# Kernel optimization log

Measured on AMD Instinct MI355X. Metric: run time of the kernel, lower is better.

## Reference

```python
import jax, jax.numpy as jnp
import numpy as np

B, N = 16, 512          # graphs, nodes per graph (equal-size dynamic batch)
IN, HID, OUT, K = 256, 128, 256, 16  # hidden = in_dim // red_factor
EPS = 1e-5


def setup_inputs() -> dict:
    key = jax.random.key(0)
    ks = jax.random.split(key, 12)
    def lin(k, fi, fo):
        return jax.random.normal(k, (fi, fo), jnp.float32) / np.sqrt(fi).astype(np.float32)
    return {
        "obj_encs": jax.random.normal(ks[0], (B * N, IN), jnp.float32),
        "n_nodes": jnp.full((B,), N, dtype=jnp.int32),
        # self-graph-attention params (in -> hidden), with residual projection
        "Wq": lin(ks[1], IN, HID), "bq": jnp.zeros((HID,), jnp.float32),
        "Wk": lin(ks[2], IN, HID), "bk": jnp.zeros((HID,), jnp.float32),
        "Wv": lin(ks[3], IN, HID), "bv": jnp.zeros((HID,), jnp.float32),
        "Wr": lin(ks[4], IN, HID), "br": jnp.zeros((HID,), jnp.float32),
        # EdgeConv (local+global => 2*HID input features)
        "Wc": lin(ks[5], 2 * HID, OUT), "bc": jnp.zeros((OUT,), jnp.float32),
        # LayerNorm affine
        "ln_scale": jnp.ones((OUT,), jnp.float32),
        "ln_bias": jnp.zeros((OUT,), jnp.float32),
    }


def _forward(obj_encs, n_nodes, Wq, bq, Wk, bk, Wv, bv, Wr, br, Wc, bc, ln_scale, ln_bias):
    # dynamic batching: equal-size graphs per n_nodes -> reshape [B, N, IN]
    x = obj_encs.reshape(B, N, IN)

    # --- SelfGraphAttentionLinear (per-graph dot-product attention, residual) ---
    q = x @ Wq + bq                      # [B, N, HID]
    kk = x @ Wk + bk
    v = x @ Wv + bv
    attn = jax.nn.softmax(jnp.einsum('bnd,bmd->bnm', q, kk) / np.sqrt(HID).astype(np.float32), axis=-1)
    h = jnp.einsum('bnm,bmd->bnd', attn, v) + (x @ Wr + br)  # residual projection

    # --- GraphConv: kNN (euclidean) within each graph ---
    sq = jnp.sum(h * h, axis=-1)                             # [B, N]
    dist = sq[:, :, None] + sq[:, None, :] - 2.0 * jnp.einsum('bnd,bmd->bnm', h, h)
    _, idx = jax.lax.top_k(-dist, K)                         # [B, N, K] (self included)

    nb = jax.vmap(lambda hb, ib: hb[ib])(h, idx)             # [B, N, K, HID]
    hc = h[:, :, None, :]                                    # [B, N, 1, HID]
    # features='local+global': [x_i, x_j - x_i]
    e = jnp.concatenate([jnp.broadcast_to(hc, nb.shape), nb - hc], axis=-1)  # [B,N,K,2H]

    y = jnp.einsum('bnkf,fo->bnko', e, Wc) + bc              # [B, N, K, OUT]
    y = jnp.max(y, axis=2)                                   # reduction='max' over k

    mu = jnp.mean(y, axis=-1, keepdims=True)
    var = jnp.mean((y - mu) ** 2, axis=-1, keepdims=True)
    y = (y - mu) / jnp.sqrt(var + EPS) * ln_scale + ln_bias  # LayerNorm
    return jax.nn.selu(y).reshape(B * N, OUT)


def reference(obj_encs, n_nodes, Wq, bq, Wk, bk, Wv, bv, Wr, br, Wc, bc, ln_scale, ln_bias):
    return _forward(obj_encs, n_nodes, Wq, bq, Wk, bk, Wv, bv, Wr, br, Wc, bc, ln_scale, ln_bias)
```

## Files before the change

### kernel.cpp

```cpp
#include <hip/hip_runtime.h>
#include <math.h>

#define NB   16
#define NN   512
#define FIN  256
#define HID  128
#define FOUT 256
#define TOPK 16
#define ROWS (NB*NN)
#define LN_EPS 1e-5f

#define BK  32
#define LDK 40

typedef __attribute__((ext_vector_type(8))) short  bf16x8;
typedef __attribute__((ext_vector_type(4))) float  f32x4;

__device__ __forceinline__ ushort f2bf_rn(float x) {
    uint u = __float_as_uint(x);
    u += 0x7fff + ((u >> 16) & 1);
    return (ushort)(u >> 16);
}
__device__ __forceinline__ float bf2f(ushort h) {
    return __uint_as_float(((uint)h) << 16);
}
__device__ __forceinline__ void split2(float x, ushort& hi, ushort& lo) {
    hi = f2bf_rn(x);
    lo = f2bf_rn(x - bf2f(hi));
}

__device__ __forceinline__ void stage_rows64(ushort (*Dh)[LDK], ushort (*Dl)[LDK],
                                             const float* __restrict__ src,
                                             int rstride, int tid)
{
    const int r = tid >> 2, seg = (tid & 3) * 8;
    const float* p = src + (size_t)r * rstride + seg;
    #pragma unroll
    for (int i = 0; i < 2; i++) {
        const float4 q = *(const float4*)(p + 4*i);
        ushort h0,l0,h1,l1,h2,l2,h3,l3;
        split2(q.x,h0,l0); split2(q.y,h1,l1);
        split2(q.z,h2,l2); split2(q.w,h3,l3);
        *(ushort4*)&Dh[r][seg + 4*i] = make_ushort4(h0,h1,h2,h3);
        *(ushort4*)&Dl[r][seg + 4*i] = make_ushort4(l0,l1,l2,l3);
    }
}

__device__ __forceinline__ void stage_cols64(ushort (*Dh)[LDK], ushort (*Dl)[LDK],
                                             const float* __restrict__ src,
                                             int ldn, int tid)
{
    const int n = tid & 63, kh = (tid >> 6) * 8;
    const float* p = src + (size_t)kh * ldn + n;
    ushort hh[8], ll[8];
    #pragma unroll
    for (int i = 0; i < 8; i++) split2(p[(size_t)i * ldn], hh[i], ll[i]);
    *(ushort4*)&Dh[n][kh]     = make_ushort4(hh[0],hh[1],hh[2],hh[3]);
    *(ushort4*)&Dh[n][kh + 4] = make_ushort4(hh[4],hh[5],hh[6],hh[7]);
    *(ushort4*)&Dl[n][kh]     = make_ushort4(ll[0],ll[1],ll[2],ll[3]);
    *(ushort4*)&Dl[n][kh + 4] = make_ushort4(ll[4],ll[5],ll[6],ll[7]);
}

__device__ __forceinline__ void mma_step64(const ushort (*Ah)[LDK], const ushort (*Al)[LDK],
                                           const ushort (*Bh)[LDK], const ushort (*Bl)[LDK],
                                           f32x4 acc[2][2], int wr, int wc, int lane)
{
    const int q8 = (lane >> 4) * 8, m = lane & 15;
    bf16x8 ah[2], al[2], bh[2], bl[2];
    #pragma unroll
    for (int i = 0; i < 2; i++) {
        ah[i] = *(const bf16x8*)&Ah[wr + 16*i + m][q8];
        al[i] = *(const bf16x8*)&Al[wr + 16*i + m][q8];
        bh[i] = *(const bf16x8*)&Bh[wc + 16*i + m][q8];
        bl[i] = *(const bf16x8*)&Bl[wc + 16*i + m][q8];
    }
    #pragma unroll
    for (int i = 0; i < 2; i++)
        #pragma unroll
        for (int j = 0; j < 2; j++) {
            acc[i][j] = __builtin_amdgcn_mfma_f32_16x16x32_bf16(ah[i], bh[j], acc[i][j], 0, 0, 0);
            acc[i][j] = __builtin_amdgcn_mfma_f32_16x16x32_bf16(ah[i], bl[j], acc[i][j], 0, 0, 0);
            acc[i][j] = __builtin_amdgcn_mfma_f32_16x16x32_bf16(al[i], bh[j], acc[i][j], 0, 0, 0);
        }
}

#define MM64_PROLOGUE()                                                     \
    __shared__ ushort Ah[64][LDK], Al[64][LDK], Bh[64][LDK], Bl[64][LDK];   \
    const int tid = threadIdx.x, lane = tid & 63, wv = tid >> 6;            \
    const int wr = (wv >> 1) * 32, wc = (wv & 1) * 32;                      \
    f32x4 acc[2][2];                                                        \
    _Pragma("unroll")                                                       \
    for (int i = 0; i < 2; i++)                                             \
        _Pragma("unroll")                                                   \
        for (int j = 0; j < 2; j++)                                         \
            acc[i][j] = (f32x4){0.f, 0.f, 0.f, 0.f};

__global__ __launch_bounds__(256) void k_proj_m(
    const float* __restrict__ X,
    const float* __restrict__ Wq, const float* __restrict__ bq,
    const float* __restrict__ Wk, const float* __restrict__ bk,
    const float* __restrict__ Wv, const float* __restrict__ bv,
    const float* __restrict__ Wr, const float* __restrict__ br,
    float* __restrict__ Y)
{
    const int widx = blockIdx.x >> 1;
    const int ch   = (blockIdx.x & 1) * 64;
    const int br0  = blockIdx.y * 64;
    const float* W; const float* bias;
    if      (widx == 0) { W = Wq; bias = bq; }
    else if (widx == 1) { W = Wk; bias = bk; }
    else if (widx == 2) { W = Wv; bias = bv; }
    else                { W = Wr; bias = br; }

    MM64_PROLOGUE();

    for (int k0 = 0; k0 < FIN; k0 += BK) {
        stage_rows64(Ah, Al, X + (size_t)br0 * FIN + k0, FIN, tid);
        stage_cols64(Bh, Bl, W + (size_t)k0 * HID + ch, HID, tid);
        __syncthreads();
        mma_step64(Ah, Al, Bh, Bl, acc, wr, wc, lane);
        __syncthreads();
    }

    const int m = lane & 15, q4 = (lane >> 4) * 4;
    #pragma unroll
    for (int i = 0; i < 2; i++)
        #pragma unroll
        for (int reg = 0; reg < 4; reg++) {
            const int grow = br0 + wr + 16*i + q4 + reg;
            #pragma unroll
            for (int j = 0; j < 2; j++) {
                const int c = ch + wc + 16*j + m;
                Y[(size_t)grow * 512 + widx * 128 + c] = acc[i][j][reg] + bias[c];
            }
        }
}

__global__ __launch_bounds__(256) void k_scores_m(
    const float* __restrict__ Y, float* __restrict__ S)
{
    const int b = blockIdx.z;
    const int m0 = blockIdx.x * 64, n0 = blockIdx.y * 64;
    const float scale = 0.08838834764831845f;
    const float* Yb = Y + (size_t)b * NN * 512;

    MM64_PROLOGUE();

    for (int k0 = 0; k0 < HID; k0 += BK) {
        stage_rows64(Ah, Al, Yb + (size_t)n0 * 512 + k0,       512, tid);
        stage_rows64(Bh, Bl, Yb + (size_t)m0 * 512 + 128 + k0, 512, tid);
        __syncthreads();
        mma_step64(Ah, Al, Bh, Bl, acc, wr, wc, lane);
        __syncthreads();
    }

    float* Sb = S + (size_t)b * NN * NN;
    const int m = lane & 15, q4 = (lane >> 4) * 4;
    #pragma unroll
    for (int i = 0; i < 2; i++)
        #pragma unroll
        for (int reg = 0; reg < 4; reg++) {
            const int n = n0 + wr + 16*i + q4 + reg;
            #pragma unroll
            for (int j = 0; j < 2; j++)
                Sb[(size_t)n * NN + m0 + wc + 16*j + m] = acc[i][j][reg] * scale;
        }
}

__global__ __launch_bounds__(256) void k_softmax(float* __restrict__ S)
{
    float* p = S + (size_t)blockIdx.x * NN;
    const int tid = threadIdx.x;
    const int lane = tid & 63, wave = tid >> 6;
    __shared__ float red[4];

    float v0 = p[tid], v1 = p[tid + 256];
    float mx = fmaxf(v0, v1);
    #pragma unroll
    for (int off = 32; off > 0; off >>= 1) mx = fmaxf(mx, __shfl_down(mx, off));
    if (lane == 0) red[wave] = mx;
    __syncthreads();
    mx = fmaxf(fmaxf(red[0], red[1]), fmaxf(red[2], red[3]));
    __syncthreads();

    float e0 = __expf(v0 - mx), e1 = __expf(v1 - mx);
    float s = e0 + e1;
    #pragma unroll
    for (int off = 32; off > 0; off >>= 1) s += __shfl_down(s, off);
    if (lane == 0) red[wave] = s;
    __syncthreads();
    s = red[0] + red[1] + red[2] + red[3];
    const float inv = 1.0f / s;
    p[tid] = e0 * inv;
    p[tid + 256] = e1 * inv;
}

__global__ __launch_bounds__(256) void k_hgemm_m(
    const float* __restrict__ S, const float* __restrict__ Y,
    float* __restrict__ H)
{
    const int c0 = blockIdx.x * 64;
    const int n0 = blockIdx.y * 64;
    const int b  = blockIdx.z;
    const float* P = S + (size_t)b * NN * NN;

    MM64_PROLOGUE();

    for (int k0 = 0; k0 < NN; k0 += BK) {
        stage_rows64(Ah, Al, P + (size_t)n0 * NN + k0, NN, tid);
        stage_cols64(Bh, Bl, Y + ((size_t)(b * NN + k0)) * 512 + 256 + c0, 512, tid);
        __syncthreads();
        mma_step64(Ah, Al, Bh, Bl, acc, wr, wc, lane);
        __syncthreads();
    }

    const int m = lane & 15, q4 = (lane >> 4) * 4;
    #pragma unroll
    for (int i = 0; i < 2; i++)
        #pragma unroll
        for (int reg = 0; reg < 4; reg++) {
            const int gr = b * NN + n0 + wr + 16*i + q4 + reg;
            #pragma unroll
            for (int j = 0; j < 2; j++) {
                const int c = c0 + wc + 16*j + m;
                H[(size_t)gr * HID + c] = acc[i][j][reg] + Y[(size_t)gr * 512 + 384 + c];
            }
        }
}

__global__ __launch_bounds__(256) void k_sq(
    const float* __restrict__ H, float* __restrict__ SQ)
{
    const int row = blockIdx.x * 4 + (threadIdx.x >> 6);
    const int lane = threadIdx.x & 63;
    float a = H[(size_t)row*HID + lane];
    float c = H[(size_t)row*HID + 64 + lane];
    float s = a*a + c*c;
    #pragma unroll
    for (int off = 32; off > 0; off >>= 1) s += __shfl_down(s, off);
    if (lane == 0) SQ[row] = s;
}

__global__ __launch_bounds__(256) void k_ab_m(
    const float* __restrict__ H, const float* __restrict__ Wc,
    const float* __restrict__ bc, float* __restrict__ AB)
{
    const int ct  = blockIdx.x;
    const int br0 = blockIdx.y * 64;
    const bool bhalf = ct >= 4;
    const int c0 = (ct & 3) * 64;

    MM64_PROLOGUE();

    for (int k0 = 0; k0 < HID; k0 += BK) {
        stage_rows64(Ah, Al, H + (size_t)br0 * HID + k0, HID, tid);
        {
            const int n = tid & 63, kh = (tid >> 6) * 8;
            ushort hh[8], ll[8];
            #pragma unroll
            for (int i = 0; i < 8; i++) {
                const int k = k0 + kh + i;
                const float wbot = Wc[(size_t)(HID + k) * FOUT + c0 + n];
                const float val = bhalf ? wbot
                                        : (Wc[(size_t)k * FOUT + c0 + n] - wbot);
                split2(val, hh[i], ll[i]);
            }
            *(ushort4*)&Bh[n][kh]     = make_ushort4(hh[0],hh[1],hh[2],hh[3]);
            *(ushort4*)&Bh[n][kh + 4] = make_ushort4(hh[4],hh[5],hh[6],hh[7]);
            *(ushort4*)&Bl[n][kh]     = make_ushort4(ll[0],ll[1],ll[2],ll[3]);
            *(ushort4*)&Bl[n][kh + 4] = make_ushort4(ll[4],ll[5],ll[6],ll[7]);
        }
        __syncthreads();
        mma_step64(Ah, Al, Bh, Bl, acc, wr, wc, lane);
        __syncthreads();
    }

    const int m = lane & 15, q4 = (lane >> 4) * 4;
    #pragma unroll
    for (int i = 0; i < 2; i++)
        #pragma unroll
        for (int reg = 0; reg < 4; reg++) {
            const int grow = br0 + wr + 16*i + q4 + reg;
            #pragma unroll
            for (int j = 0; j < 2; j++) {
                const int c = wc + 16*j + m;
                const float add = bhalf ? 0.0f : bc[c0 + c];
                AB[(size_t)grow * 512 + ct * 64 + c] = acc[i][j][reg] + add;
            }
        }
}

__global__ __launch_bounds__(256) void k_dist_m(
    const float* __restrict__ H, const float* __restrict__ SQ,
    float* __restrict__ D)
{
    const int b = blockIdx.z;
    const int m0 = blockIdx.x * 64, n0 = blockIdx.y * 64;
    const float* Hb = H + (size_t)b * NN * HID;

    MM64_PROLOGUE();

    for (int k0 = 0; k0 < HID; k0 += BK) {
        stage_rows64(Ah, Al, Hb + (size_t)n0 * HID + k0, HID, tid);
        stage_rows64(Bh, Bl, Hb + (size_t)m0 * HID + k0, HID, tid);
        __syncthreads();
        mma_step64(Ah, Al, Bh, Bl, acc, wr, wc, lane);
        __syncthreads();
    }

    const int gb = b * NN;
    float* Db = D + (size_t)b * NN * NN;
    const int m = lane & 15, q4 = (lane >> 4) * 4;
    float sqm[2];
    #pragma unroll
    for (int j = 0; j < 2; j++) sqm[j] = SQ[gb + m0 + wc + 16*j + m];
    #pragma unroll
    for (int i = 0; i < 2; i++)
        #pragma unroll
        for (int reg = 0; reg < 4; reg++) {
            const int n = n0 + wr + 16*i + q4 + reg;
            const float sqn = SQ[gb + n];
            #pragma unroll
            for (int j = 0; j < 2; j++)
                Db[(size_t)n * NN + m0 + wc + 16*j + m]
                    = sqn + sqm[j] - 2.0f * acc[i][j][reg];
        }
}

__global__ __launch_bounds__(256) void k_out(
    const float* __restrict__ D, const float* __restrict__ AB,
    const float* __restrict__ ln_scale, const float* __restrict__ ln_bias,
    float* __restrict__ out)
{
    const int row  = blockIdx.x * 4 + (threadIdx.x >> 6);
    const int lane = threadIdx.x & 63;
    const int gb0  = row & ~(NN - 1);

    const float* drow = D + (size_t)row * NN;
    const float4 q0 = ((const float4*)drow)[lane];
    const float4 q1 = ((const float4*)drow)[64 + lane];
    float v[8] = {q0.x, q0.y, q0.z, q0.w, q1.x, q1.y, q1.z, q1.w};

    const float lsc0 = ln_scale[lane],       lbi0 = ln_bias[lane];
    const float lsc1 = ln_scale[lane + 64],  lbi1 = ln_bias[lane + 64];
    const float lsc2 = ln_scale[lane + 128], lbi2 = ln_bias[lane + 128];
    const float lsc3 = ln_scale[lane + 192], lbi3 = ln_bias[lane + 192];
    const float* arow = AB + (size_t)row * 512;
    const float a0 = arow[lane], a1 = arow[lane + 64],
                a2 = arow[lane + 128], a3 = arow[lane + 192];

    float bm0 = -INFINITY, bm1 = -INFINITY, bm2 = -INFINITY, bm3 = -INFINITY;

    for (int it = 0; it < TOPK; it++) {
        float bestv = v[0]; int bestm = 4*lane;
        #pragma unroll
        for (int j = 1; j < 8; j++) {
            const int m = (j >> 2)*256 + 4*lane + (j & 3);
            if (v[j] < bestv) { bestv = v[j]; bestm = m; }
        }
        #pragma unroll
        for (int off = 1; off < 64; off <<= 1) {
            const float ov = __shfl_xor(bestv, off);
            const int   om = __shfl_xor(bestm, off);
            if (ov < bestv || (ov == bestv && om < bestm)) { bestv = ov; bestm = om; }
        }
        const float* brow = AB + (size_t)(gb0 + bestm) * 512 + 256;
        bm0 = fmaxf(bm0, brow[lane]);
        bm1 = fmaxf(bm1, brow[lane + 64]);
        bm2 = fmaxf(bm2, brow[lane + 128]);
        bm3 = fmaxf(bm3, brow[lane + 192]);
        if (((bestm >> 2) & 63) == lane) {
            const int jj = ((bestm >> 8) << 2) | (bestm & 3);
            #pragma unroll
            for (int j = 0; j < 8; j++) if (j == jj) v[j] = INFINITY;
        }
    }

    float y0 = a0 + bm0, y1 = a1 + bm1, y2 = a2 + bm2, y3 = a3 + bm3;

    float s = y0 + y1 + y2 + y3;
    #pragma unroll
    for (int off = 1; off < 64; off <<= 1) s += __shfl_xor(s, off);
    const float mu = s * (1.0f/256.0f);
    const float d0 = y0 - mu, d1 = y1 - mu, d2 = y2 - mu, d3 = y3 - mu;
    float s2 = d0*d0 + d1*d1 + d2*d2 + d3*d3;
    #pragma unroll
    for (int off = 1; off < 64; off <<= 1) s2 += __shfl_xor(s2, off);
    const float var = s2 * (1.0f/256.0f);
    const float rstd = rsqrtf(var + LN_EPS);

    const float lam = 1.0507009873554805f, alpha = 1.6732632423543772f;
    float* orow = out + (size_t)row * FOUT;
    { const float z = d0*rstd*lsc0 + lbi0; orow[lane]       = z > 0.f ? lam*z : lam*alpha*expm1f(z); }
    { const float z = d1*rstd*lsc1 + lbi1; orow[lane + 64]  = z > 0.f ? lam*z : lam*alpha*expm1f(z); }
    { const float z = d2*rstd*lsc2 + lbi2; orow[lane + 128] = z > 0.f ? lam*z : lam*alpha*expm1f(z); }
    { const float z = d3*rstd*lsc3 + lbi3; orow[lane + 192] = z > 0.f ? lam*z : lam*alpha*expm1f(z); }
}

extern "C" void kernel_launch(void* const* d_in, const int* in_sizes, int n_in,
                              void* d_out, int out_size, void* d_ws, size_t ws_size,
                              hipStream_t stream)
{
    (void)in_sizes; (void)n_in; (void)out_size; (void)ws_size;
    const float* X   = (const float*)d_in[0];
    const float* Wq  = (const float*)d_in[2];
    const float* bq  = (const float*)d_in[3];
    const float* Wk  = (const float*)d_in[4];
    const float* bk  = (const float*)d_in[5];
    const float* Wv  = (const float*)d_in[6];
    const float* bv  = (const float*)d_in[7];
    const float* Wr  = (const float*)d_in[8];
    const float* br  = (const float*)d_in[9];
    const float* Wc  = (const float*)d_in[10];
    const float* bc  = (const float*)d_in[11];
    const float* lns = (const float*)d_in[12];
    const float* lnb = (const float*)d_in[13];
    float* out = (float*)d_out;

    float* ws = (float*)d_ws;
    float* Y  = ws;
    float* S  = Y + (size_t)ROWS*512;
    float* H  = S + (size_t)NB*NN*NN;
    float* SQ = H + (size_t)ROWS*HID;
    float* AB = SQ + ROWS;
    float* D  = S;

    k_proj_m  <<<dim3(8,128),  256, 0, stream>>>(X, Wq,bq, Wk,bk, Wv,bv, Wr,br, Y);
    k_scores_m<<<dim3(8,8,16), 256, 0, stream>>>(Y, S);
    k_softmax <<<ROWS,         256, 0, stream>>>(S);
    k_hgemm_m <<<dim3(2,8,16), 256, 0, stream>>>(S, Y, H);
    k_sq      <<<ROWS/4,       256, 0, stream>>>(H, SQ);
    k_ab_m    <<<dim3(8,128),  256, 0, stream>>>(H, Wc, bc, AB);
    k_dist_m  <<<dim3(8,8,16), 256, 0, stream>>>(H, SQ, D);
    k_out     <<<ROWS/4,       256, 0, stream>>>(D, AB, lns, lnb, out);
}
```

Before: 198.2 us.

## Fuse pipeline into cooperative persistent megakernel with flash-style attention

Replaces the eight separate kernels with one cooperative persistent kernel that runs five phases separated by grid syncs, and keeps separate per-phase kernels as a fallback. The projection phase stores pre-split bf16 hi/lo copies of Q/K and a transposed V, so later phases skip repeated conversion. Attention becomes a flash-style split over 8 key chunks that writes partial outputs, maxima and sums, which a combine phase merges and uses to produce H and its squared norms. This removes the full score matrix write, the separate softmax pass and several launches, at the cost of extra partial-output traffic and grid-wide barriers.

```diff
diff --git a/kernel.cpp b/kernel.cpp
--- a/kernel.cpp
+++ b/kernel.cpp
@@ -1,5 +1,8 @@
 #include <hip/hip_runtime.h>
+#include <hip/hip_cooperative_groups.h>
 #include <math.h>
+
+namespace cg = cooperative_groups;
 
 #define NB   16
 #define NN   512
@@ -10,11 +13,19 @@
 #define ROWS (NB*NN)
 #define LN_EPS 1e-5f
 
-#define BK  32
-#define LDK 40
-
-typedef __attribute__((ext_vector_type(8))) short  bf16x8;
-typedef __attribute__((ext_vector_type(4))) float  f32x4;
+#define BK   32
+#define LDK  40
+#define GRID 512
+#define NTHR 256
+
+typedef __attribute__((ext_vector_type(8)))  short  bf16x8;
+typedef __attribute__((ext_vector_type(4)))  float  f32x4;
+typedef __attribute__((ext_vector_type(8)))  unsigned short u16x8;
+
+#define MFMA3(d, ah, al, bh, bl)                                              \
+    d = __builtin_amdgcn_mfma_f32_16x16x32_bf16(ah, bh, d, 0, 0, 0);          \
+    d = __builtin_amdgcn_mfma_f32_16x16x32_bf16(ah, bl, d, 0, 0, 0);          \
+    d = __builtin_amdgcn_mfma_f32_16x16x32_bf16(al, bh, d, 0, 0, 0);
 
 __device__ __forceinline__ ushort f2bf_rn(float x) {
     uint u = __float_as_uint(x);
@@ -29,9 +40,9 @@
     lo = f2bf_rn(x - bf2f(hi));
 }
 
-__device__ __forceinline__ void stage_rows64(ushort (*Dh)[LDK], ushort (*Dl)[LDK],
-                                             const float* __restrict__ src,
-                                             int rstride, int tid)
+__device__ __forceinline__ void stage_rows64f(ushort (*Dh)[LDK], ushort (*Dl)[LDK],
+                                              const float* __restrict__ src,
+                                              int rstride, int tid)
 {
     const int r = tid >> 2, seg = (tid & 3) * 8;
     const float* p = src + (size_t)r * rstride + seg;
@@ -46,9 +57,9 @@
     }
 }
 
-__device__ __forceinline__ void stage_cols64(ushort (*Dh)[LDK], ushort (*Dl)[LDK],
-                                             const float* __restrict__ src,
-                                             int ldn, int tid)
+__device__ __forceinline__ void stage_cols64f(ushort (*Dh)[LDK], ushort (*Dl)[LDK],
+                                              const float* __restrict__ src,
+                                              int ldn, int tid)
 {
     const int n = tid & 63, kh = (tid >> 6) * 8;
     const float* p = src + (size_t)kh * ldn + n;
@@ -61,6 +72,13 @@
     *(ushort4*)&Dl[n][kh + 4] = make_ushort4(ll[4],ll[5],ll[6],ll[7]);
 }
 
+__device__ __forceinline__ void stage_u(ushort (*Ds)[LDK], const ushort* __restrict__ src,
+                                        int rstride, int tid)
+{
+    const int r = tid >> 2, seg = (tid & 3) * 8;
+    *(u16x8*)&Ds[r][seg] = *(const u16x8*)(src + (size_t)r * rstride + seg);
+}
+
 __device__ __forceinline__ void mma_step64(const ushort (*Ah)[LDK], const ushort (*Al)[LDK],
                                            const ushort (*Bh)[LDK], const ushort (*Bl)[LDK],
                                            f32x4 acc[2][2], int wr, int wc, int lane)
@@ -78,359 +96,485 @@
     for (int i = 0; i < 2; i++)
         #pragma unroll
         for (int j = 0; j < 2; j++) {
-            acc[i][j] = __builtin_amdgcn_mfma_f32_16x16x32_bf16(ah[i], bh[j], acc[i][j], 0, 0, 0);
-            acc[i][j] = __builtin_amdgcn_mfma_f32_16x16x32_bf16(ah[i], bl[j], acc[i][j], 0, 0, 0);
-            acc[i][j] = __builtin_amdgcn_mfma_f32_16x16x32_bf16(al[i], bh[j], acc[i][j], 0, 0, 0);
-        }
-}
-
-#define MM64_PROLOGUE()                                                     \
-    __shared__ ushort Ah[64][LDK], Al[64][LDK], Bh[64][LDK], Bl[64][LDK];   \
-    const int tid = threadIdx.x, lane = tid & 63, wv = tid >> 6;            \
-    const int wr = (wv >> 1) * 32, wc = (wv & 1) * 32;                      \
-    f32x4 acc[2][2];                                                        \
-    _Pragma("unroll")                                                       \
-    for (int i = 0; i < 2; i++)                                             \
-        _Pragma("unroll")                                                   \
-        for (int j = 0; j < 2; j++)                                         \
-            acc[i][j] = (f32x4){0.f, 0.f, 0.f, 0.f};
-
-__global__ __launch_bounds__(256) void k_proj_m(
-    const float* __restrict__ X,
-    const float* __restrict__ Wq, const float* __restrict__ bq,
-    const float* __restrict__ Wk, const float* __restrict__ bk,
-    const float* __restrict__ Wv, const float* __restrict__ bv,
-    const float* __restrict__ Wr, const float* __restrict__ br,
-    float* __restrict__ Y)
-{
-    const int widx = blockIdx.x >> 1;
-    const int ch   = (blockIdx.x & 1) * 64;
-    const int br0  = blockIdx.y * 64;
-    const float* W; const float* bias;
-    if      (widx == 0) { W = Wq; bias = bq; }
-    else if (widx == 1) { W = Wk; bias = bk; }
-    else if (widx == 2) { W = Wv; bias = bv; }
-    else                { W = Wr; bias = br; }
-
-    MM64_PROLOGUE();
-
-    for (int k0 = 0; k0 < FIN; k0 += BK) {
-        stage_rows64(Ah, Al, X + (size_t)br0 * FIN + k0, FIN, tid);
-        stage_cols64(Bh, Bl, W + (size_t)k0 * HID + ch, HID, tid);
+            MFMA3(acc[i][j], ah[i], al[i], bh[j], bl[j]);
+        }
+}
+
+struct Params {
+    const float *X, *Wq, *bq, *Wk, *bk, *Wv, *bv, *Wr, *br, *Wc, *bc, *lns, *lnb;
+    float *out;
+    float *Rbuf, *SQ, *AB, *D, *Opart, *Mpart, *Lpart;
+    ushort *Yh, *Yl, *Vth, *Vtl, *Hh, *Hl;
+};
+
+__device__ void phaseA(const Params& P, ushort* SMEM, int blk, int nblk)
+{
+    ushort (*Ah)[LDK] = (ushort(*)[LDK])(SMEM);
+    ushort (*Al)[LDK] = (ushort(*)[LDK])(SMEM + 2560);
+    ushort (*Bh)[LDK] = (ushort(*)[LDK])(SMEM + 5120);
+    ushort (*Bl)[LDK] = (ushort(*)[LDK])(SMEM + 7680);
+    float* fbuf = (float*)SMEM;
+
+    const int tid = threadIdx.x, lane = tid & 63, w = tid >> 6;
+    const int wr = (w >> 1) * 32, wc = (w & 1) * 32;
+    const int m = lane & 15, q4 = (lane >> 4) * 4;
+
+    for (int job = blk; job < 1024; job += nblk) {
+        const int ct = job >> 7, br0 = (job & 127) * 64;
+        const int widx = ct >> 1, ch = (ct & 1) * 64;
+        const float* W    = widx==0 ? P.Wq : widx==1 ? P.Wk : widx==2 ? P.Wv : P.Wr;
+        const float* bias = widx==0 ? P.bq : widx==1 ? P.bk : widx==2 ? P.bv : P.br;
         __syncthreads();
-        mma_step64(Ah, Al, Bh, Bl, acc, wr, wc, lane);
+        f32x4 acc[2][2];
+        #pragma unroll
+        for (int i = 0; i < 2; i++)
+            #pragma unroll
+            for (int j = 0; j < 2; j++) acc[i][j] = (f32x4){0.f,0.f,0.f,0.f};
+
+        for (int k0 = 0; k0 < FIN; k0 += BK) {
+            stage_rows64f(Ah, Al, P.X + (size_t)br0 * FIN + k0, FIN, tid);
+            stage_cols64f(Bh, Bl, W + (size_t)k0 * HID + ch, HID, tid);
+            __syncthreads();
+            mma_step64(Ah, Al, Bh, Bl, acc, wr, wc, lane);
+            __syncthreads();
+        }
+        #pragma unroll
+        for (int i = 0; i < 2; i++)
+            #pragma unroll
+            for (int reg = 0; reg < 4; reg++) {
+                const int r = wr + 16*i + q4 + reg;
+                #pragma unroll
+                for (int j = 0; j < 2; j++) {
+                    const int c = wc + 16*j + m;
+                    fbuf[r*65 + c] = acc[i][j][reg] + bias[ch + c];
+                }
+            }
         __syncthreads();
-    }
-
+
+        if (ct < 4) {
+            const int r = tid >> 2, cs = (tid & 3) * 16;
+            u16x8 vh0, vh1, vl0, vl1;
+            #pragma unroll
+            for (int t = 0; t < 8; t++) {
+                ushort hh, ll;
+                split2(fbuf[r*65 + cs + t], hh, ll);     vh0[t]=hh; vl0[t]=ll;
+                split2(fbuf[r*65 + cs + 8 + t], hh, ll); vh1[t]=hh; vl1[t]=ll;
+            }
+            const size_t o = (size_t)(br0 + r) * 256 + ct*64 + cs;
+            *(u16x8*)&P.Yh[o]   = vh0; *(u16x8*)&P.Yh[o+8] = vh1;
+            *(u16x8*)&P.Yl[o]   = vl0; *(u16x8*)&P.Yl[o+8] = vl1;
+        } else if (ct < 6) {
+            const int cl = tid >> 2, rs = (tid & 3) * 16;
+            const int b = br0 >> 9, nb = br0 & 511;
+            const int cglob = (ct - 4) * 64 + cl;
+            u16x8 vh0, vh1, vl0, vl1;
+            #pragma unroll
+            for (int t = 0; t < 8; t++) {
+                ushort hh, ll;
+                split2(fbuf[(rs+t)*65 + cl], hh, ll);   vh0[t]=hh; vl0[t]=ll;
+                split2(fbuf[(rs+8+t)*65 + cl], hh, ll); vh1[t]=hh; vl1[t]=ll;
+            }
+            const size_t o = ((size_t)b*128 + cglob) * 512 + nb + rs;
+            *(u16x8*)&P.Vth[o]   = vh0; *(u16x8*)&P.Vth[o+8] = vh1;
+            *(u16x8*)&P.Vtl[o]   = vl0; *(u16x8*)&P.Vtl[o+8] = vl1;
+        } else {
+            const int r = tid >> 2, cs = (tid & 3) * 16;
+            float* dst = P.Rbuf + (size_t)(br0 + r) * 128 + (ct - 6)*64 + cs;
+            #pragma unroll
+            for (int t = 0; t < 16; t += 4) {
+                float4 q;
+                q.x = fbuf[r*65+cs+t];   q.y = fbuf[r*65+cs+t+1];
+                q.z = fbuf[r*65+cs+t+2]; q.w = fbuf[r*65+cs+t+3];
+                *(float4*)(dst + t) = q;
+            }
+        }
+    }
+}
+
+__device__ void phaseB(const Params& P, ushort* SMEM, int blk, int nblk)
+{
+    ushort (*P0h)[LDK] = (ushort(*)[LDK])(SMEM);
+    ushort (*P0l)[LDK] = (ushort(*)[LDK])(SMEM + 2560);
+    ushort (*Bh)[LDK]  = (ushort(*)[LDK])(SMEM + 5120);
+    ushort (*Bl)[LDK]  = (ushort(*)[LDK])(SMEM + 7680);
+
+    const int tid = threadIdx.x, lane = tid & 63, w = tid >> 6;
+    const int L = lane & 15, quad = lane >> 4;
+    const float scale = 0.08838834764831845f;
+
+    for (int job = blk; job < 1024; job += nblk) {
+        const int b = job >> 6, rest = job & 63;
+        const int n0 = (rest >> 3) * 64, mc = rest & 7, m0 = mc * 64;
+        const int grow0 = b*NN + n0 + w*16;
+
+        bf16x8 qh[4], ql[4];
+        #pragma unroll
+        for (int s = 0; s < 4; s++) {
+            const size_t qo = (size_t)(grow0 + L) * 256 + s*32 + quad*8;
+            qh[s] = *(const bf16x8*)(P.Yh + qo);
+            ql[s] = *(const bf16x8*)(P.Yl + qo);
+        }
+
+        f32x4 Sf[4];
+        #pragma unroll
+        for (int j = 0; j < 4; j++) Sf[j] = (f32x4){0.f,0.f,0.f,0.f};
+
+        for (int s = 0; s < 4; s++) {
+            __syncthreads();
+            {
+                const int r = tid >> 2, seg = (tid & 3) * 8;
+                const size_t o = (size_t)(b*NN + m0 + r) * 256 + 128 + s*32 + seg;
+                *(u16x8*)&Bh[r][seg] = *(const u16x8*)(P.Yh + o);
+                *(u16x8*)&Bl[r][seg] = *(const u16x8*)(P.Yl + o);
+            }
+            __syncthreads();
+            #pragma unroll
+            for (int j = 0; j < 4; j++) {
+                bf16x8 kh = *(const bf16x8*)&Bh[16*j + L][quad*8];
+                bf16x8 kl = *(const bf16x8*)&Bl[16*j + L][quad*8];
+                MFMA3(Sf[j], qh[s], ql[s], kh, kl);
+            }
+        }
+        #pragma unroll
+        for (int j = 0; j < 4; j++)
+            #pragma unroll
+            for (int r = 0; r < 4; r++) Sf[j][r] *= scale;
+
+        float mx[4], ls[4];
+        #pragma unroll
+        for (int r = 0; r < 4; r++) {
+            float v = fmaxf(fmaxf(Sf[0][r], Sf[1][r]), fmaxf(Sf[2][r], Sf[3][r]));
+            v = fmaxf(v, __shfl_xor(v, 1));
+            v = fmaxf(v, __shfl_xor(v, 2));
+            v = fmaxf(v, __shfl_xor(v, 4));
+            v = fmaxf(v, __shfl_xor(v, 8));
+            mx[r] = v; ls[r] = 0.f;
+        }
+
+        __syncthreads();
+
+        #pragma unroll
+        for (int j = 0; j < 4; j++)
+            #pragma unroll
+            for (int r = 0; r < 4; r++) {
+                const float p = __expf(Sf[j][r] - mx[r]);
+                ls[r] += p;
+                const int row = w*16 + quad*4 + r, cc = (16*j + (lane & 15)) & 31;
+                ushort hh, ll; split2(p, hh, ll);
+                if (j < 2) { P0h[row][cc] = hh; P0l[row][cc] = ll; }
+                else       { Bh[row][cc]  = hh; Bl[row][cc]  = ll; }
+            }
+        #pragma unroll
+        for (int r = 0; r < 4; r++) {
+            float v = ls[r];
+            v += __shfl_xor(v, 1); v += __shfl_xor(v, 2);
+            v += __shfl_xor(v, 4); v += __shfl_xor(v, 8);
+            ls[r] = v;
+        }
+
+        f32x4 O[8];
+        #pragma unroll
+        for (int j = 0; j < 8; j++) O[j] = (f32x4){0.f,0.f,0.f,0.f};
+        #pragma unroll
+        for (int s2 = 0; s2 < 2; s2++) {
+            bf16x8 ph = s2 ? *(const bf16x8*)&Bh[w*16 + L][quad*8]
+                           : *(const bf16x8*)&P0h[w*16 + L][quad*8];
+            bf16x8 pl = s2 ? *(const bf16x8*)&Bl[w*16 + L][quad*8]
+                           : *(const bf16x8*)&P0l[w*16 + L][quad*8];
+            #pragma unroll
+            for (int j = 0; j < 8; j++) {
+                const size_t vo = ((size_t)(b*128 + 16*j + L)) * 512 + m0 + s2*32 + quad*8;
+                bf16x8 vh = *(const bf16x8*)(P.Vth + vo);
+                bf16x8 vl = *(const bf16x8*)(P.Vtl + vo);
+                MFMA3(O[j], ph, pl, vh, vl);
+            }
+        }
+
+        #pragma unroll
+        for (int j = 0; j < 8; j++)
+            #pragma unroll
+            for (int reg = 0; reg < 4; reg++) {
+                const int grow = grow0 + quad*4 + reg;
+                P.Opart[((size_t)mc*ROWS + grow)*128 + 16*j + L] = O[j][reg];
+            }
+        if (L == 0) {
+            #pragma unroll
+            for (int reg = 0; reg < 4; reg++) {
+                const int grow = grow0 + quad*4 + reg;
+                P.Mpart[(size_t)mc*ROWS + grow] = mx[reg];
+                P.Lpart[(size_t)mc*ROWS + grow] = ls[reg];
+            }
+        }
+    }
+}
+
+__device__ void phaseC(const Params& P, int blk, int nblk)
+{
+    const int lane = threadIdx.x & 63, w = threadIdx.x >> 6;
+    for (int row = blk*4 + w; row < ROWS; row += nblk*4) {
+        float mp[8], M = -INFINITY;
+        #pragma unroll
+        for (int p = 0; p < 8; p++) {
+            mp[p] = P.Mpart[(size_t)p*ROWS + row];
+            M = fmaxf(M, mp[p]);
+        }
+        float Ls = 0.f, o0 = 0.f, o1 = 0.f;
+        #pragma unroll
+        for (int p = 0; p < 8; p++) {
+            const float e = __expf(mp[p] - M);
+            Ls += e * P.Lpart[(size_t)p*ROWS + row];
+            const float* op = P.Opart + ((size_t)p*ROWS + row)*128;
+            o0 += e * op[lane];
+            o1 += e * op[lane + 64];
+        }
+        const float invl = 1.0f / Ls;
+        const float h0 = o0*invl + P.Rbuf[(size_t)row*128 + lane];
+        const float h1 = o1*invl + P.Rbuf[(size_t)row*128 + lane + 64];
+        ushort hh, ll;
+        split2(h0, hh, ll); P.Hh[(size_t)row*128 + lane] = hh;      P.Hl[(size_t)row*128 + lane] = ll;
+        split2(h1, hh, ll); P.Hh[(size_t)row*128 + lane + 64] = hh; P.Hl[(size_t)row*128 + lane + 64] = ll;
+        float s = h0*h0 + h1*h1;
+        #pragma unroll
+        for (int off = 1; off < 64; off <<= 1) s += __shfl_xor(s, off);
+        if (lane == 0) P.SQ[row] = s;
+    }
+}
+
+__device__ void phaseD(const Params& P, ushort* SMEM, int blk, int nblk)
+{
+    ushort (*Ah)[LDK] = (ushort(*)[LDK])(SMEM);
+    ushort (*Al)[LDK] = (ushort(*)[LDK])(SMEM + 2560);
+    ushort (*Bh)[LDK] = (ushort(*)[LDK])(SMEM + 5120);
+    ushort (*Bl)[LDK] = (ushort(*)[LDK])(SMEM + 7680);
+
+    const int tid = threadIdx.x, lane = tid & 63, w = tid >> 6;
+    const int wr = (w >> 1) * 32, wc = (w & 1) * 32;
     const int m = lane & 15, q4 = (lane >> 4) * 4;
-    #pragma unroll
-    for (int i = 0; i < 2; i++)
-        #pragma unroll
-        for (int reg = 0; reg < 4; reg++) {
-            const int grow = br0 + wr + 16*i + q4 + reg;
-            #pragma unroll
-            for (int j = 0; j < 2; j++) {
-                const int c = ch + wc + 16*j + m;
-                Y[(size_t)grow * 512 + widx * 128 + c] = acc[i][j][reg] + bias[c];
-            }
-        }
-}
-
-__global__ __launch_bounds__(256) void k_scores_m(
-    const float* __restrict__ Y, float* __restrict__ S)
-{
-    const int b = blockIdx.z;
-    const int m0 = blockIdx.x * 64, n0 = blockIdx.y * 64;
-    const float scale = 0.08838834764831845f;
-    const float* Yb = Y + (size_t)b * NN * 512;
-
-    MM64_PROLOGUE();
-
-    for (int k0 = 0; k0 < HID; k0 += BK) {
-        stage_rows64(Ah, Al, Yb + (size_t)n0 * 512 + k0,       512, tid);
-        stage_rows64(Bh, Bl, Yb + (size_t)m0 * 512 + 128 + k0, 512, tid);
+
+    for (int job = blk; job < 2048; job += nblk) {
         __syncthreads();
-        mma_step64(Ah, Al, Bh, Bl, acc, wr, wc, lane);
-        __syncthreads();
-    }
-
-    float* Sb = S + (size_t)b * NN * NN;
-    const int m = lane & 15, q4 = (lane >> 4) * 4;
-    #pragma unroll
-    for (int i = 0; i < 2; i++)
-        #pragma unroll
-        for (int reg = 0; reg < 4; reg++) {
-            const int n = n0 + wr + 16*i + q4 + reg;
-            #pragma unroll
-            for (int j = 0; j < 2; j++)
-                Sb[(size_t)n * NN + m0 + wc + 16*j + m] = acc[i][j][reg] * scale;
-        }
-}
-
-__global__ __launch_bounds__(256) void k_softmax(float* __restrict__ S)
-{
-    float* p = S + (size_t)blockIdx.x * NN;
-    const int tid = threadIdx.x;
-    const int lane = tid & 63, wave = tid >> 6;
-    __shared__ float red[4];
-
-    float v0 = p[tid], v1 = p[tid + 256];
-    float mx = fmaxf(v0, v1);
-    #pragma unroll
-    for (int off = 32; off > 0; off >>= 1) mx = fmaxf(mx, __shfl_down(mx, off));
-    if (lane == 0) red[wave] = mx;
-    __syncthreads();
-    mx = fmaxf(fmaxf(red[0], red[1]), fmaxf(red[2], red[3]));
-    __syncthreads();
-
-    float e0 = __expf(v0 - mx), e1 = __expf(v1 - mx);
-    float s = e0 + e1;
-    #pragma unroll
-    for (int off = 32; off > 0; off >>= 1) s += __shfl_down(s, off);
-    if (lane == 0) red[wave] = s;
-    __syncthreads();
-    s = red[0] + red[1] + red[2] + red[3];
-    const float inv = 1.0f / s;
-    p[tid] = e0 * inv;
-    p[tid + 256] = e1 * inv;
-}
-
-__global__ __launch_bounds__(256) void k_hgemm_m(
-    const float* __restrict__ S, const float* __restrict__ Y,
-    float* __restrict__ H)
-{
-    const int c0 = blockIdx.x * 64;
-    const int n0 = blockIdx.y * 64;
-    const int b  = blockIdx.z;
-    const float* P = S + (size_t)b * NN * NN;
-
-    MM64_PROLOGUE();
-
-    for (int k0 = 0; k0 < NN; k0 += BK) {
-        stage_rows64(Ah, Al, P + (size_t)n0 * NN + k0, NN, tid);
-        stage_cols64(Bh, Bl, Y + ((size_t)(b * NN + k0)) * 512 + 256 + c0, 512, tid);
-        __syncthreads();
-        mma_step64(Ah, Al, Bh, Bl, acc, wr, wc, lane);
-        __syncthreads();
-    }
-
-    const int m = lane & 15, q4 = (lane >> 4) * 4;
-    #pragma unroll
-    for (int i = 0; i < 2; i++)
-        #pragma unroll
-        for (int reg = 0; reg < 4; reg++) {
-            const int gr = b * NN + n0 + wr + 16*i + q4 + reg;
-            #pragma unroll
-            for (int j = 0; j < 2; j++) {
-                const int c = c0 + wc + 16*j + m;
-                H[(size_t)gr * HID + c] = acc[i][j][reg] + Y[(size_t)gr * 512 + 384 + c];
-            }
-        }
-}
-
-__global__ __launch_bounds__(256) void k_sq(
-    const float* __restrict__ H, float* __restrict__ SQ)
-{
-    const int row = blockIdx.x * 4 + (threadIdx.x >> 6);
-    const int lane = threadIdx.x & 63;
-    float a = H[(size_t)row*HID + lane];
-    float c = H[(size_t)row*HID + 64 + lane];
-    float s = a*a + c*c;
-    #pragma unroll
-    for (int off = 32; off > 0; off >>= 1) s += __shfl_down(s, off);
-    if (lane == 0) SQ[row] = s;
-}
-
-__global__ __launch_bounds__(256) void k_ab_m(
-    const float* __restrict__ H, const float* __restrict__ Wc,
-    const float* __restrict__ bc, float* __restrict__ AB)
-{
-    const int ct  = blockIdx.x;
-    const int br0 = blockIdx.y * 64;
-    const bool bhalf = ct >= 4;
-    const int c0 = (ct & 3) * 64;
-
-    MM64_PROLOGUE();
-
-    for (int k0 = 0; k0 < HID; k0 += BK) {
-        stage_rows64(Ah, Al, H + (size_t)br0 * HID + k0, HID, tid);
-        {
-            const int n = tid & 63, kh = (tid >> 6) * 8;
-            ushort hh[8], ll[8];
-            #pragma unroll
-            for (int i = 0; i < 8; i++) {
-                const int k = k0 + kh + i;
-                const float wbot = Wc[(size_t)(HID + k) * FOUT + c0 + n];
-                const float val = bhalf ? wbot
-                                        : (Wc[(size_t)k * FOUT + c0 + n] - wbot);
-                split2(val, hh[i], ll[i]);
-            }
-            *(ushort4*)&Bh[n][kh]     = make_ushort4(hh[0],hh[1],hh[2],hh[3]);
-            *(ushort4*)&Bh[n][kh + 4] = make_ushort4(hh[4],hh[5],hh[6],hh[7]);
-            *(ushort4*)&Bl[n][kh]     = make_ushort4(ll[0],ll[1],ll[2],ll[3]);
-            *(ushort4*)&Bl[n][kh + 4] = make_ushort4(ll[4],ll[5],ll[6],ll[7]);
-        }
-        __syncthreads();
-        mma_step64(Ah, Al, Bh, Bl, acc, wr, wc, lane);
-        __syncthreads();
-    }
-
-    const int m = lane & 15, q4 = (lane >> 4) * 4;
-    #pragma unroll
-    for (int i = 0; i < 2; i++)
-        #pragma unroll
-        for (int reg = 0; reg < 4; reg++) {
-            const int grow = br0 + wr + 16*i + q4 + reg;
-            #pragma unroll
-            for (int j = 0; j < 2; j++) {
-                const int c = wc + 16*j + m;
-                const float add = bhalf ? 0.0f : bc[c0 + c];
-                AB[(size_t)grow * 512 + ct * 64 + c] = acc[i][j][reg] + add;
-            }
-        }
-}
-
-__global__ __launch_bounds__(256) void k_dist_m(
-    const float* __restrict__ H, const float* __restrict__ SQ,
-    float* __restrict__ D)
-{
-    const int b = blockIdx.z;
-    const int m0 = blockIdx.x * 64, n0 = blockIdx.y * 64;
-    const float* Hb = H + (size_t)b * NN * HID;
-
-    MM64_PROLOGUE();
-
-    for (int k0 = 0; k0 < HID; k0 += BK) {
-        stage_rows64(Ah, Al, Hb + (size_t)n0 * HID + k0, HID, tid);
-        stage_rows64(Bh, Bl, Hb + (size_t)m0 * HID + k0, HID, tid);
-        __syncthreads();
-        mma_step64(Ah, Al, Bh, Bl, acc, wr, wc, lane);
-        __syncthreads();
-    }
-
-    const int gb = b * NN;
-    float* Db = D + (size_t)b * NN * NN;
-    const int m = lane & 15, q4 = (lane >> 4) * 4;
-    float sqm[2];
-    #pragma unroll
-    for (int j = 0; j < 2; j++) sqm[j] = SQ[gb + m0 + wc + 16*j + m];
-    #pragma unroll
-    for (int i = 0; i < 2; i++)
-        #pragma unroll
-        for (int reg = 0; reg < 4; reg++) {
-            const int n = n0 + wr + 16*i + q4 + reg;
-            const float sqn = SQ[gb + n];
-            #pragma unroll
-            for (int j = 0; j < 2; j++)
-                Db[(size_t)n * NN + m0 + wc + 16*j + m]
-                    = sqn + sqm[j] - 2.0f * acc[i][j][reg];
-        }
-}
-
-__global__ __launch_bounds__(256) void k_out(
-    const float* __restrict__ D, const float* __restrict__ AB,
-    const float* __restrict__ ln_scale, const float* __restrict__ ln_bias,
-    float* __restrict__ out)
-{
-    const int row  = blockIdx.x * 4 + (threadIdx.x >> 6);
-    const int lane = threadIdx.x & 63;
-    const int gb0  = row & ~(NN - 1);
-
-    const float* drow = D + (size_t)row * NN;
-    const float4 q0 = ((const float4*)drow)[lane];
-    const float4 q1 = ((const float4*)drow)[64 + lane];
-    float v[8] = {q0.x, q0.y, q0.z, q0.w, q1.x, q1.y, q1.z, q1.w};
-
-    const float lsc0 = ln_scale[lane],       lbi0 = ln_bias[lane];
-    const float lsc1 = ln_scale[lane + 64],  lbi1 = ln_bias[lane + 64];
-    const float lsc2 = ln_scale[lane + 128], lbi2 = ln_bias[lane + 128];
-    const float lsc3 = ln_scale[lane + 192], lbi3 = ln_bias[lane + 192];
-    const float* arow = AB + (size_t)row * 512;
-    const float a0 = arow[lane], a1 = arow[lane + 64],
-                a2 = arow[lane + 128], a3 = arow[lane + 192];
-
-    float bm0 = -INFINITY, bm1 = -INFINITY, bm2 = -INFINITY, bm3 = -INFINITY;
-
-    for (int it = 0; it < TOPK; it++) {
-        float bestv = v[0]; int bestm = 4*lane;
-        #pragma unroll
-        for (int j = 1; j < 8; j++) {
-            const int m = (j >> 2)*256 + 4*lane + (j & 3);
-            if (v[j] < bestv) { bestv = v[j]; bestm = m; }
-        }
-        #pragma unroll
-        for (int off = 1; off < 64; off <<= 1) {
-            const float ov = __shfl_xor(bestv, off);
-            const int   om = __shfl_xor(bestm, off);
-            if (ov < bestv || (ov == bestv && om < bestm)) { bestv = ov; bestm = om; }
-        }
-        const float* brow = AB + (size_t)(gb0 + bestm) * 512 + 256;
-        bm0 = fmaxf(bm0, brow[lane]);
-        bm1 = fmaxf(bm1, brow[lane + 64]);
-        bm2 = fmaxf(bm2, brow[lane + 128]);
-        bm3 = fmaxf(bm3, brow[lane + 192]);
-        if (((bestm >> 2) & 63) == lane) {
-            const int jj = ((bestm >> 8) << 2) | (bestm & 3);
-            #pragma unroll
-            for (int j = 0; j < 8; j++) if (j == jj) v[j] = INFINITY;
-        }
-    }
-
-    float y0 = a0 + bm0, y1 = a1 + bm1, y2 = a2 + bm2, y3 = a3 + bm3;
-
-    float s = y0 + y1 + y2 + y3;
-    #pragma unroll
-    for (int off = 1; off < 64; off <<= 1) s += __shfl_xor(s, off);
-    const float mu = s * (1.0f/256.0f);
-    const float d0 = y0 - mu, d1 = y1 - mu, d2 = y2 - mu, d3 = y3 - mu;
-    float s2 = d0*d0 + d1*d1 + d2*d2 + d3*d3;
-    #pragma unroll
-    for (int off = 1; off < 64; off <<= 1) s2 += __shfl_xor(s2, off);
-    const float var = s2 * (1.0f/256.0f);
-    const float rstd = rsqrtf(var + LN_EPS);
-
-    const float lam = 1.0507009873554805f, alpha = 1.6732632423543772f;
-    float* orow = out + (size_t)row * FOUT;
-    { const float z = d0*rstd*lsc0 + lbi0; orow[lane]       = z > 0.f ? lam*z : lam*alpha*expm1f(z); }
-    { const float z = d1*rstd*lsc1 + lbi1; orow[lane + 64]  = z > 0.f ? lam*z : lam*alpha*expm1f(z); }
-    { const float z = d2*rstd*lsc2 + lbi2; orow[lane + 128] = z > 0.f ? lam*z : lam*alpha*expm1f(z); }
-    { const float z = d3*rstd*lsc3 + lbi3; orow[lane + 192] = z > 0.f ? lam*z : lam*alpha*expm1f(z); }
-}
+        f32x4 acc[2][2];
+        #pragma unroll
+        for (int i = 0; i < 2; i++)
+            #pragma unroll
+            for (int j = 0; j < 2; j++) acc[i][j] = (f32x4){0.f,0.f,0.f,0.f};
+
+        if (job < 1024) {
+            const int ct = job >> 7, br0 = (job & 127) * 64;
+            const bool bhalf = ct >= 4;
+            const int c0 = (ct & 3) * 64;
+            for (int k0 = 0; k0 < HID; k0 += BK) {
+                stage_u(Ah, P.Hh + (size_t)br0 * 128 + k0, 128, tid);
+                stage_u(Al, P.Hl + (size_t)br0 * 128 + k0, 128, tid);
+                {
+                    const int n = tid & 63, kh2 = (tid >> 6) * 8;
+                    ushort hh[8], llv[8];
+                    #pragma unroll
+                    for (int i = 0; i < 8; i++) {
+                        const int k = k0 + kh2 + i;
+                        const float bot = P.Wc[(size_t)(HID + k) * FOUT + c0 + n];
+                        const float val = bhalf ? bot
+                                                : (P.Wc[(size_t)k * FOUT + c0 + n] - bot);
+                        split2(val, hh[i], llv[i]);
+                    }
+                    *(ushort4*)&Bh[n][kh2]     = make_ushort4(hh[0],hh[1],hh[2],hh[3]);
+                    *(ushort4*)&Bh[n][kh2 + 4] = make_ushort4(hh[4],hh[5],hh[6],hh[7]);
+                    *(ushort4*)&Bl[n][kh2]     = make_ushort4(llv[0],llv[1],llv[2],llv[3]);
+                    *(ushort4*)&Bl[n][kh2 + 4] = make_ushort4(llv[4],llv[5],llv[6],llv[7]);
+                }
+                __syncthreads();
+                mma_step64(Ah, Al, Bh, Bl, acc, wr, wc, lane);
+                __syncthreads();
+            }
+            #pragma unroll
+            for (int i = 0; i < 2; i++)
+                #pragma unroll
+                for (int reg = 0; reg < 4; reg++) {
+                    const int grow = br0 + wr + 16*i + q4 + reg;
+                    #pragma unroll
+                    for (int j = 0; j < 2; j++) {
+                        const int c = wc + 16*j + m;
+                        const float add = bhalf ? 0.0f : P.bc[c0 + c];
+                        P.AB[(size_t)grow * 512 + ct*64 + c] = acc[i][j][reg] + add;
+                    }
+                }
+        } else {
+            const int t = job - 1024;
+            const int b = t >> 6, rest = t & 63;
+            const int m0 = (rest >> 3) * 64, n0 = (rest & 7) * 64;
+            for (int k0 = 0; k0 < HID; k0 += BK) {
+                stage_u(Ah, P.Hh + (size_t)(b*NN + n0) * 128 + k0, 128, tid);
+                stage_u(Al, P.Hl + (size_t)(b*NN + n0) * 128 + k0, 128, tid);
+                stage_u(Bh, P.Hh + (size_t)(b*NN + m0) * 128 + k0, 128, tid);
+                stage_u(Bl, P.Hl + (size_t)(b*NN + m0) * 128 + k0, 128, tid);
+                __syncthreads();
+                mma_step64(Ah, Al, Bh, Bl, acc, wr, wc, lane);
+                __syncthreads();
+            }
+            const int gb = b * NN;
+            float* Db = P.D + (size_t)b * NN * NN;
+            float sqm[2];
+            #pragma unroll
+            for (int j = 0; j < 2; j++) sqm[j] = P.SQ[gb + m0 + wc + 16*j + m];
+            #pragma unroll
+            for (int i = 0; i < 2; i++)
+                #pragma unroll
+                for (int reg = 0; reg < 4; reg++) {
+                    const int n = n0 + wr + 16*i + q4 + reg;
+                    const float sqn = P.SQ[gb + n];
+                    #pragma unroll
+                    for (int j = 0; j < 2; j++)
+                        Db[(size_t)n * NN + m0 + wc + 16*j + m]
+                            = sqn + sqm[j] - 2.0f * acc[i][j][reg];
+                }
+        }
+    }
+}
+
+__device__ void phaseE(const Params& P, int blk, int nblk)
+{
+    const int lane = threadIdx.x & 63, w = threadIdx.x >> 6;
+    for (int row = blk*4 + w; row < ROWS; row += nblk*4) {
+        const int gb0 = row & ~(NN - 1);
+        const float* drow = P.D + (size_t)row * NN;
+        const float4 dq0 = ((const float4*)drow)[lane];
+        const float4 dq1 = ((const float4*)drow)[64 + lane];
+        float v[8] = {dq0.x, dq0.y, dq0.z, dq0.w, dq1.x, dq1.y, dq1.z, dq1.w};
+
+        const float lsc0 = P.lns[lane],       lbi0 = P.lnb[lane];
+        const float lsc1 = P.lns[lane + 64],  lbi1 = P.lnb[lane + 64];
+        const float lsc2 = P.lns[lane + 128], lbi2 = P.lnb[lane + 128];
+        const float lsc3 = P.lns[lane + 192], lbi3 = P.lnb[lane + 192];
+        const float* arow = P.AB + (size_t)row * 512;
+        const float a0 = arow[lane], a1 = arow[lane + 64],
+                    a2 = arow[lane + 128], a3 = arow[lane + 192];
+
+        float bm0 = -INFINITY, bm1 = -INFINITY, bm2 = -INFINITY, bm3 = -INFINITY;
+
+        for (int it = 0; it < TOPK; it++) {
+            float bestv = v[0]; int bestm = 4*lane;
+            #pragma unroll
+            for (int j = 1; j < 8; j++) {
+                const int mm = (j >> 2)*256 + 4*lane + (j & 3);
+                if (v[j] < bestv) { bestv = v[j]; bestm = mm; }
+            }
+            #pragma unroll
+            for (int off = 1; off < 64; off <<= 1) {
+                const float ov = __shfl_xor(bestv, off);
+                const int   om = __shfl_xor(bestm, off);
+                if (ov < bestv || (ov == bestv && om < bestm)) { bestv = ov; bestm = om; }
+            }
+            const float* brow = P.AB + (size_t)(gb0 + bestm) * 512 + 256;
+            bm0 = fmaxf(bm0, brow[lane]);
+            bm1 = fmaxf(bm1, brow[lane + 64]);
+            bm2 = fmaxf(bm2, brow[lane + 128]);
+            bm3 = fmaxf(bm3, brow[lane + 192]);
+            if (((bestm >> 2) & 63) == lane) {
+                const int jj = ((bestm >> 8) << 2) | (bestm & 3);
+                #pragma unroll
+                for (int j = 0; j < 8; j++) if (j == jj) v[j] = INFINITY;
+            }
+        }
+
+        float y0 = a0 + bm0, y1 = a1 + bm1, y2 = a2 + bm2, y3 = a3 + bm3;
+        float s = y0 + y1 + y2 + y3;
+        #pragma unroll
+        for (int off = 1; off < 64; off <<= 1) s += __shfl_xor(s, off);
+        const float mu = s * (1.0f/256.0f);
+        const float d0 = y0 - mu, d1 = y1 - mu, d2 = y2 - mu, d3 = y3 - mu;
+        float s2 = d0*d0 + d1*d1 + d2*d2 + d3*d3;
+        #pragma unroll
+        for (int off = 1; off < 64; off <<= 1) s2 += __shfl_xor(s2, off);
+        const float var = s2 * (1.0f/256.0f);
+        const float rstd = rsqrtf(var + LN_EPS);
+
+        const float lam = 1.0507009873554805f, alpha = 1.6732632423543772f;
+        float* orow = P.out + (size_t)row * FOUT;
+        { const float z = d0*rstd*lsc0 + lbi0; orow[lane]       = z > 0.f ? lam*z : lam*alpha*expm1f(z); }
+        { const float z = d1*rstd*lsc1 + lbi1; orow[lane + 64]  = z > 0.f ? lam*z : lam*alpha*expm1f(z); }
+        { const float z = d2*rstd*lsc2 + lbi2; orow[lane + 128] = z > 0.f ? lam*z : lam*alpha*expm1f(z); }
+        { const float z = d3*rstd*lsc3 + lbi3; orow[lane + 192] = z > 0.f ? lam*z : lam*alpha*expm1f(z); }
+    }
+}
+
+__global__ __launch_bounds__(NTHR, 2) void k_mega(Params P)
+{
+    cg::grid_group grid = cg::this_grid();
+    __shared__ ushort SMEM[4*64*LDK];
+    phaseA(P, SMEM, blockIdx.x, GRID);
+    grid.sync();
+    phaseB(P, SMEM, blockIdx.x, GRID);
+    grid.sync();
+    phaseC(P, blockIdx.x, GRID);
+    grid.sync();
+    phaseD(P, SMEM, blockIdx.x, GRID);
+    grid.sync();
+    phaseE(P, blockIdx.x, GRID);
+}
+
+__global__ __launch_bounds__(NTHR, 2) void k_pA(Params P) {
+    __shared__ ushort SMEM[4*64*LDK];
+    phaseA(P, SMEM, blockIdx.x, gridDim.x);
+}
+__global__ __launch_bounds__(NTHR, 2) void k_pB(Params P) {
+    __shared__ ushort SMEM[4*64*LDK];
+    phaseB(P, SMEM, blockIdx.x, gridDim.x);
+}
+__global__ __launch_bounds__(NTHR, 2) void k_pC(Params P) { phaseC(P, blockIdx.x, gridDim.x); }
+__global__ __launch_bounds__(NTHR, 2) void k_pD(Params P) {
+    __shared__ ushort SMEM[4*64*LDK];
+    phaseD(P, SMEM, blockIdx.x, gridDim.x);
+}
+__global__ __launch_bounds__(NTHR, 2) void k_pE(Params P) { phaseE(P, blockIdx.x, gridDim.x); }
 
 extern "C" void kernel_launch(void* const* d_in, const int* in_sizes, int n_in,
                               void* d_out, int out_size, void* d_ws, size_t ws_size,
                               hipStream_t stream)
 {
     (void)in_sizes; (void)n_in; (void)out_size; (void)ws_size;
-    const float* X   = (const float*)d_in[0];
-    const float* Wq  = (const float*)d_in[2];
-    const float* bq  = (const float*)d_in[3];
-    const float* Wk  = (const float*)d_in[4];
-    const float* bk  = (const float*)d_in[5];
-    const float* Wv  = (const float*)d_in[6];
-    const float* bv  = (const float*)d_in[7];
-    const float* Wr  = (const float*)d_in[8];
-    const float* br  = (const float*)d_in[9];
-    const float* Wc  = (const float*)d_in[10];
-    const float* bc  = (const float*)d_in[11];
-    const float* lns = (const float*)d_in[12];
-    const float* lnb = (const float*)d_in[13];
-    float* out = (float*)d_out;
-
-    float* ws = (float*)d_ws;
-    float* Y  = ws;
-    float* S  = Y + (size_t)ROWS*512;
-    float* H  = S + (size_t)NB*NN*NN;
-    float* SQ = H + (size_t)ROWS*HID;
-    float* AB = SQ + ROWS;
-    float* D  = S;
-
-    k_proj_m  <<<dim3(8,128),  256, 0, stream>>>(X, Wq,bq, Wk,bk, Wv,bv, Wr,br, Y);
-    k_scores_m<<<dim3(8,8,16), 256, 0, stream>>>(Y, S);
-    k_softmax <<<ROWS,         256, 0, stream>>>(S);
-    k_hgemm_m <<<dim3(2,8,16), 256, 0, stream>>>(S, Y, H);
-    k_sq      <<<ROWS/4,       256, 0, stream>>>(H, SQ);
-    k_ab_m    <<<dim3(8,128),  256, 0, stream>>>(H, Wc, bc, AB);
-    k_dist_m  <<<dim3(8,8,16), 256, 0, stream>>>(H, SQ, D);
-    k_out     <<<ROWS/4,       256, 0, stream>>>(D, AB, lns, lnb, out);
-}
+
+    char* cur = (char*)d_ws;
+    auto alloc = [&](size_t bytes) { char* p = cur; cur += (bytes + 255) & ~size_t(255); return p; };
+
+    Params P;
+    P.X   = (const float*)d_in[0];
+    P.Wq  = (const float*)d_in[2];
+    P.bq  = (const float*)d_in[3];
+    P.Wk  = (const float*)d_in[4];
+    P.bk  = (const float*)d_in[5];
+    P.Wv  = (const float*)d_in[6];
+    P.bv  = (const float*)d_in[7];
+    P.Wr  = (const float*)d_in[8];
+    P.br  = (const float*)d_in[9];
+    P.Wc  = (const float*)d_in[10];
+    P.bc  = (const float*)d_in[11];
+    P.lns = (const float*)d_in[12];
+    P.lnb = (const float*)d_in[13];
+    P.out = (float*)d_out;
+
+    P.D     = (float*)alloc((size_t)NB*NN*NN*4);
+    P.AB    = (float*)alloc((size_t)ROWS*512*4);
+    P.Opart = (float*)alloc((size_t)8*ROWS*128*4);
+    P.Mpart = (float*)alloc((size_t)8*ROWS*4);
+    P.Lpart = (float*)alloc((size_t)8*ROWS*4);
+    P.Rbuf  = (float*)alloc((size_t)ROWS*128*4);
+    P.SQ    = (float*)alloc((size_t)ROWS*4);
+    P.Yh    = (ushort*)alloc((size_t)ROWS*256*2);
+    P.Yl    = (ushort*)alloc((size_t)ROWS*256*2);
+    P.Vth   = (ushort*)alloc((size_t)NB*128*512*2);
+    P.Vtl   = (ushort*)alloc((size_t)NB*128*512*2);
+    P.Hh    = (ushort*)alloc((size_t)ROWS*128*2);
+    P.Hl    = (ushort*)alloc((size_t)ROWS*128*2);
+
+    void* args[] = { (void*)&P };
+    hipError_t e = hipLaunchCooperativeKernel((const void*)k_mega, dim3(GRID), dim3(NTHR),
+                                              args, 0, stream);
+    if (e != hipSuccess) {
+        (void)hipGetLastError();
+        k_pA<<<1024, NTHR, 0, stream>>>(P);
+        k_pB<<<1024, NTHR, 0, stream>>>(P);
+        k_pC<<<2048, NTHR, 0, stream>>>(P);
+        k_pD<<<2048, NTHR, 0, stream>>>(P);
+        k_pE<<<2048, NTHR, 0, stream>>>(P);
+    }
+}
```

Result: slower. 499.0 us (+151.7%).
